# Optimization experiments

Measured on AMD Instinct MI355X. Metric: run time of the kernel, lower is better.

Reference implementation:

```python
import jax, jax.numpy as jnp
import numpy as np

SIZE = 32
NUM_CLASSES = 10
B = 16384
RTOL = 0.01
ATOL = 0.01
MAX_STEPS = 96
H0 = 0.05


def setup_inputs() -> dict:
    key = jax.random.key(0)
    ks = jax.random.split(key, 9)
    p = lambda k, s: 0.1 * jax.random.normal(k, s, dtype=jnp.float32)
    z = lambda n: jnp.zeros((n,), dtype=jnp.float32)
    x = jax.random.normal(ks[0], (B, 2), dtype=jnp.float32)
    # per-sample ODE end times T_i in (0, 3]
    samples = 3.0 * jax.random.uniform(ks[1], (B, 1), dtype=jnp.float32) + 1e-3
    return dict(
        x=x, samples=samples,
        node_w1=p(ks[2], (3, SIZE)), node_b1=z(SIZE),
        node_w2=p(ks[3], (SIZE, SIZE)), node_b2=z(SIZE),
        node_w3=p(ks[4], (SIZE, 2)), node_b3=z(2),
        fc_w=p(ks[5], (2, NUM_CLASSES)), fc_b=z(NUM_CLASSES),
        enc_w1=p(ks[6], (2, SIZE)), enc_b1=z(SIZE),
        enc_w2=p(ks[7], (SIZE, SIZE)), enc_b2=z(SIZE),
        enc_w3=p(ks[8], (SIZE, 2)), enc_b3=z(2),
    )


def _net_forward(x, samples, node_w1, node_b1, node_w2, node_b2, node_w3, node_b3,
                 fc_w, fc_b, enc_w1, enc_b1, enc_w2, enc_b2, enc_w3, enc_b3):
    # Encoder -> (alpha, beta) feed only the external prob_model (no effect on act_vec)
    h = jax.nn.relu(x @ enc_w1 + enc_b1)
    h = jax.nn.relu(h @ enc_w2 + enc_b2)
    ab = h @ enc_w3 + enc_b3
    alpha, beta = jnp.exp(ab[:, 0]), jnp.exp(ab[:, 1])  # unused downstream (side effects only)

    # samples[samples >= 50] = 50
    T = jnp.minimum(samples[:, 0], 50.0)  # [B] per-sample end times

    def f(t, y):  # NODE dynamics; t: [B], y: [B,2]
        zin = jnp.concatenate([t[:, None], y], axis=1)  # [B,3]
        h1 = jax.nn.relu(zin @ node_w1 + node_b1)
        h2 = jax.nn.relu(h1 @ node_w2 + node_b2)
        return h2 @ node_w3 + node_b3  # [B,2]

    def step(carry, _):
        t, y, hstep = carry
        rem = T - t
        active = rem > 1e-8
        hs = jnp.where(active, jnp.minimum(hstep, rem), 0.0)  # never overshoot T
        hb = hs[:, None]
        # Dopri5 (RK45) stages
        k1 = f(t, y)
        k2 = f(t + hs * 0.2, y + hb * (0.2 * k1))
        k3 = f(t + hs * 0.3, y + hb * (3.0 / 40.0 * k1 + 9.0 / 40.0 * k2))
        k4 = f(t + hs * 0.8, y + hb * (44.0 / 45.0 * k1 - 56.0 / 15.0 * k2 + 32.0 / 9.0 * k3))
        k5 = f(t + hs * (8.0 / 9.0), y + hb * (19372.0 / 6561.0 * k1 - 25360.0 / 2187.0 * k2 + 64448.0 / 6561.0 * k3 - 212.0 / 729.0 * k4))
        k6 = f(t + hs, y + hb * (9017.0 / 3168.0 * k1 - 355.0 / 33.0 * k2 + 46732.0 / 5247.0 * k3 + 49.0 / 176.0 * k4 - 5103.0 / 18656.0 * k5))
        y5 = y + hb * (35.0 / 384.0 * k1 + 500.0 / 1113.0 * k3 + 125.0 / 192.0 * k4 - 2187.0 / 6784.0 * k5 + 11.0 / 84.0 * k6)
        k7 = f(t + hs, y5)
        err = hb * (71.0 / 57600.0 * k1 - 71.0 / 16695.0 * k3 + 71.0 / 1920.0 * k4 - 17253.0 / 339200.0 * k5 + 22.0 / 525.0 * k6 - 1.0 / 40.0 * k7)
        scale = ATOL + RTOL * jnp.maximum(jnp.abs(y), jnp.abs(y5))
        en = jnp.sqrt(jnp.mean((err / scale) ** 2, axis=1))  # [B]
        accept = active & (en <= 1.0)
        fac = jnp.clip(0.9 * jnp.maximum(en, 1e-10) ** (-0.2), 0.2, 10.0)
        t_n = jnp.where(accept, t + hs, t)
        y_n = jnp.where(accept[:, None], y5, y)
        h_n = jnp.where(active, hs * fac, hstep)
        return (t_n, y_n, h_n), None

    t0 = jnp.zeros((x.shape[0],), dtype=x.dtype)
    h0 = jnp.full((x.shape[0],), H0, dtype=x.dtype)
    (tF, yF, hF), _ = jax.lax.scan(step, (t0, x, h0), None, length=MAX_STEPS)

    # temp[idx] = flow of x[idx] from t=0 to its own T[idx] (sort/scatter in the
    # original only routes each sample's own interpolated state back to its row)
    act = yF @ fc_w + fc_b  # [B, num_classes]
    return act[None, :, :]  # act_vec: [1, B, num_classes]


def reference(x, samples, node_w1, node_b1, node_w2, node_b2, node_w3, node_b3,
              fc_w, fc_b, enc_w1, enc_b1, enc_w2, enc_b2, enc_w3, enc_b3):
    return _net_forward(x, samples, node_w1, node_b1, node_w2, node_b2, node_w3, node_b3,
                        fc_w, fc_b, enc_w1, enc_b1, enc_w2, enc_b2, enc_w3, enc_b3)
```

## Files before the change

### kernel.cpp

```cpp
#include <hip/hip_runtime.h>
#include <math.h>


#define MAXS 96

typedef float v2f __attribute__((ext_vector_type(2)));

static __device__ __forceinline__ v2f splat(float s) { v2f v; v.x = s; v.y = s; return v; }
static __device__ __forceinline__ v2f vfma(v2f a, v2f b, v2f c) { return __builtin_elementwise_fma(a, b, c); }
static __device__ __forceinline__ v2f vrelu(v2f a) { return __builtin_elementwise_max(a, splat(0.0f)); }

template<int PAT>
static __device__ __forceinline__ float swzf(float x) {
    return __int_as_float(__builtin_amdgcn_ds_swizzle(__float_as_int(x), PAT));
}

#define GATH(j)  g[2*(j)]   = swzf<(((j) << 5) | 0x10)>(hx); \
                 g[2*(j)+1] = swzf<(((j) << 5) | 0x10)>(hy)

template<int X>
static __device__ __forceinline__ v2f redstage(v2f p) {
    v2f q; q.x = swzf<((X << 10) | 0x1f)>(p.x); q.y = swzf<((X << 10) | 0x1f)>(p.y);
    return p + q;
}

__global__ __launch_bounds__(256, 3) void node_kernel(
    const float* __restrict__ x, const float* __restrict__ samples,
    const float* __restrict__ w1, const float* __restrict__ b1,
    const float* __restrict__ w2, const float* __restrict__ b2,
    const float* __restrict__ w3, const float* __restrict__ b3,
    const float* __restrict__ fcw, const float* __restrict__ fcb,
    float* __restrict__ out, int n)
{
    const int tid  = blockIdx.x * blockDim.x + threadIdx.x;
    const int elem = tid >> 4;
    const int m    = tid & 15;
    if (elem >= n) return;

    const v2f* w1v = (const v2f*)w1;
    const v2f* b1v = (const v2f*)b1;
    const v2f* w2v = (const v2f*)w2;
    const v2f* b2v = (const v2f*)b2;
    const v2f* w3v = (const v2f*)w3;

    const v2f w1r0 = w1v[0 * 16 + m];
    const v2f w1r1 = w1v[1 * 16 + m];
    const v2f w1r2 = w1v[2 * 16 + m];
    const v2f b1c  = b1v[m];
    const v2f b2c  = b2v[m];
    const v2f w3r0 = w3v[2 * m + 0];
    const v2f w3r1 = w3v[2 * m + 1];
    const v2f b3c  = { b3[0], b3[1] };

    v2f w2c[32];
#pragma unroll
    for (int i = 0; i < 32; ++i) w2c[i] = w2v[i * 16 + m];

    v2f y = ((const v2f*)x)[elem];
    float T = fminf(samples[elem], 50.0f);
    float t = 0.0f;
    float h = 0.05f;

    auto f_eval = [&](float tt, v2f z) -> v2f {
        v2f hv = vfma(splat(tt), w1r0, vfma(splat(z.x), w1r1,
                 vfma(splat(z.y), w1r2, b1c)));
        hv = vrelu(hv);
        float hx = hv.x, hy = hv.y;

        float g[32];
        GATH(0);  GATH(1);  GATH(2);  GATH(3);
        GATH(4);  GATH(5);  GATH(6);  GATH(7);
        GATH(8);  GATH(9);  GATH(10); GATH(11);
        GATH(12); GATH(13); GATH(14); GATH(15);

        v2f acc = b2c;
#pragma unroll
        for (int i = 0; i < 32; ++i) acc = vfma(splat(g[i]), w2c[i], acc);
        acc = vrelu(acc);

        v2f p = vfma(splat(acc.x), w3r0, splat(acc.y) * w3r1);
        p = redstage<1>(p);
        p = redstage<2>(p);
        p = redstage<4>(p);
        p = redstage<8>(p);
        return p + b3c;
    };

    for (int s = 0; s < MAXS; ++s) {
        float rem = T - t;
        if (!(rem > 1e-8f)) break;
        float hs = fminf(h, rem);
        v2f hb = splat(hs);

        v2f k1 = f_eval(t, y);
        v2f k2 = f_eval(t + hs * 0.2f, vfma(hb, splat(0.2f) * k1, y));
        v2f k3 = f_eval(t + hs * 0.3f,
                 vfma(hb, vfma(splat((float)(3.0/40.0)), k1, splat((float)(9.0/40.0)) * k2), y));
        v2f k4 = f_eval(t + hs * 0.8f,
                 vfma(hb, vfma(splat((float)(44.0/45.0)), k1,
                          vfma(splat((float)(-56.0/15.0)), k2, splat((float)(32.0/9.0)) * k3)), y));
        v2f k5 = f_eval(t + hs * (float)(8.0/9.0),
                 vfma(hb, vfma(splat((float)(19372.0/6561.0)), k1,
                          vfma(splat((float)(-25360.0/2187.0)), k2,
                          vfma(splat((float)(64448.0/6561.0)), k3,
                               splat((float)(-212.0/729.0)) * k4))), y));
        v2f k6 = f_eval(t + hs,
                 vfma(hb, vfma(splat((float)(9017.0/3168.0)), k1,
                          vfma(splat((float)(-355.0/33.0)), k2,
                          vfma(splat((float)(46732.0/5247.0)), k3,
                          vfma(splat((float)(49.0/176.0)), k4,
                               splat((float)(-5103.0/18656.0)) * k5)))), y));
        v2f y5 = vfma(hb, vfma(splat((float)(35.0/384.0)), k1,
                          vfma(splat((float)(500.0/1113.0)), k3,
                          vfma(splat((float)(125.0/192.0)), k4,
                          vfma(splat((float)(-2187.0/6784.0)), k5,
                               splat((float)(11.0/84.0)) * k6)))), y);
        v2f k7 = f_eval(t + hs, y5);

        v2f err = hb * vfma(splat((float)(71.0/57600.0)), k1,
                       vfma(splat((float)(-71.0/16695.0)), k3,
                       vfma(splat((float)(71.0/1920.0)), k4,
                       vfma(splat((float)(-17253.0/339200.0)), k5,
                       vfma(splat((float)(22.0/525.0)), k6,
                            splat((float)(-1.0/40.0)) * k7)))));

        v2f ay  = __builtin_elementwise_abs(y);
        v2f ay5 = __builtin_elementwise_abs(y5);
        v2f sc  = vfma(splat(0.01f), __builtin_elementwise_max(ay, ay5), splat(0.01f));
        v2f r   = err / sc;
        float en = sqrtf(0.5f * (r.x * r.x + r.y * r.y));

        float fac = 0.9f * powf(fmaxf(en, 1e-10f), -0.2f);
        fac = fminf(fmaxf(fac, 0.2f), 10.0f);

        if (en <= 1.0f) { t += hs; y = y5; }
        h = hs * fac;
    }

    if (m < 10) {
        out[10 * elem + m] = fmaf(y.x, fcw[m], fmaf(y.y, fcw[10 + m], fcb[m]));
    }
}

extern "C" void kernel_launch(void* const* d_in, const int* in_sizes, int n_in,
                              void* d_out, int out_size, void* d_ws, size_t ws_size,
                              hipStream_t stream) {
    const float* x   = (const float*)d_in[0];
    const float* sm  = (const float*)d_in[1];
    const float* w1  = (const float*)d_in[2];
    const float* b1  = (const float*)d_in[3];
    const float* w2  = (const float*)d_in[4];
    const float* b2  = (const float*)d_in[5];
    const float* w3  = (const float*)d_in[6];
    const float* b3  = (const float*)d_in[7];
    const float* fcw = (const float*)d_in[8];
    const float* fcb = (const float*)d_in[9];
    float* out = (float*)d_out;

    int n = in_sizes[1];
    const int block = 256;
    long long threads = (long long)n * 16;
    int grid = (int)((threads + block - 1) / block);
    node_kernel<<<grid, block, 0, stream>>>(x, sm, w1, b1, w2, b2, w3, b3,
                                            fcw, fcb, out, n);
}
```

Measured before the change: 111.0 us.

## Reuse FSAL k7 as next k1, split layer-2 accumulators, pin weights in VGPRs

```diff
diff --git a/kernel.cpp b/kernel.cpp
--- a/kernel.cpp
+++ b/kernel.cpp
@@ -15,7 +15,7 @@
     return __int_as_float(__builtin_amdgcn_ds_swizzle(__float_as_int(x), PAT));
 }
 
-#define GATH(j)  g[2*(j)]   = swzf<(((j) << 5) | 0x10)>(hx); \
+#define GPAIR(j) g[2*(j)]   = swzf<(((j) << 5) | 0x10)>(hx); \
                  g[2*(j)+1] = swzf<(((j) << 5) | 0x10)>(hy)
 
 template<int X>
@@ -43,18 +43,23 @@
     const v2f* b2v = (const v2f*)b2;
     const v2f* w3v = (const v2f*)w3;
 
-    const v2f w1r0 = w1v[0 * 16 + m];
-    const v2f w1r1 = w1v[1 * 16 + m];
-    const v2f w1r2 = w1v[2 * 16 + m];
-    const v2f b1c  = b1v[m];
-    const v2f b2c  = b2v[m];
-    const v2f w3r0 = w3v[2 * m + 0];
-    const v2f w3r1 = w3v[2 * m + 1];
-    const v2f b3c  = { b3[0], b3[1] };
+    v2f w1r0 = w1v[0 * 16 + m];
+    v2f w1r1 = w1v[1 * 16 + m];
+    v2f w1r2 = w1v[2 * 16 + m];
+    v2f b1c  = b1v[m];
+    v2f b2c  = b2v[m];
+    v2f w3r0 = w3v[2 * m + 0];
+    v2f w3r1 = w3v[2 * m + 1];
+    v2f b3c  = { b3[0], b3[1] };
 
     v2f w2c[32];
 #pragma unroll
     for (int i = 0; i < 32; ++i) w2c[i] = w2v[i * 16 + m];
+
+#pragma unroll
+    for (int i = 0; i < 32; ++i) { asm volatile("" : "+v"(w2c[i])); }
+    asm volatile("" : "+v"(w1r0), "+v"(w1r1), "+v"(w1r2), "+v"(b1c), "+v"(b2c));
+    asm volatile("" : "+v"(w3r0), "+v"(w3r1));
 
     v2f y = ((const v2f*)x)[elem];
     float T = fminf(samples[elem], 50.0f);
@@ -68,15 +73,22 @@
         float hx = hv.x, hy = hv.y;
 
         float g[32];
-        GATH(0);  GATH(1);  GATH(2);  GATH(3);
-        GATH(4);  GATH(5);  GATH(6);  GATH(7);
-        GATH(8);  GATH(9);  GATH(10); GATH(11);
-        GATH(12); GATH(13); GATH(14); GATH(15);
+        v2f a0 = b2c, a1 = splat(0.0f), a2 = splat(0.0f), a3 = splat(0.0f);
 
-        v2f acc = b2c;
+        GPAIR(0);  GPAIR(1);  GPAIR(2);  GPAIR(3);
 #pragma unroll
-        for (int i = 0; i < 32; ++i) acc = vfma(splat(g[i]), w2c[i], acc);
-        acc = vrelu(acc);
+        for (int i = 0; i < 8; ++i)  a0 = vfma(splat(g[i]), w2c[i], a0);
+        GPAIR(4);  GPAIR(5);  GPAIR(6);  GPAIR(7);
+#pragma unroll
+        for (int i = 8; i < 16; ++i) a1 = vfma(splat(g[i]), w2c[i], a1);
+        GPAIR(8);  GPAIR(9);  GPAIR(10); GPAIR(11);
+#pragma unroll
+        for (int i = 16; i < 24; ++i) a2 = vfma(splat(g[i]), w2c[i], a2);
+        GPAIR(12); GPAIR(13); GPAIR(14); GPAIR(15);
+#pragma unroll
+        for (int i = 24; i < 32; ++i) a3 = vfma(splat(g[i]), w2c[i], a3);
+
+        v2f acc = vrelu((a0 + a1) + (a2 + a3));
 
         v2f p = vfma(splat(acc.x), w3r0, splat(acc.y) * w3r1);
         p = redstage<1>(p);
@@ -86,13 +98,14 @@
         return p + b3c;
     };
 
+    v2f k1 = f_eval(0.0f, y);
+
     for (int s = 0; s < MAXS; ++s) {
         float rem = T - t;
         if (!(rem > 1e-8f)) break;
         float hs = fminf(h, rem);
         v2f hb = splat(hs);
 
-        v2f k1 = f_eval(t, y);
         v2f k2 = f_eval(t + hs * 0.2f, vfma(hb, splat(0.2f) * k1, y));
         v2f k3 = f_eval(t + hs * 0.3f,
                  vfma(hb, vfma(splat((float)(3.0/40.0)), k1, splat((float)(9.0/40.0)) * k2), y));
@@ -133,7 +146,9 @@
         float fac = 0.9f * powf(fmaxf(en, 1e-10f), -0.2f);
         fac = fminf(fmaxf(fac, 0.2f), 10.0f);
 
-        if (en <= 1.0f) { t += hs; y = y5; }
+        bool accept = (en <= 1.0f);
+        if (accept) { t += hs; y = y5; }
+        k1 = accept ? k7 : k1;
         h = hs * fac;
     }
 
```

Result: no change. 110.2 us (-0.7%).
